# Performance work log

Hardware: AMD Instinct MI355X
Metric: run time of the kernel (lower is better)

## Reference

```python
import jax, jax.numpy as jnp
import numpy as np

B, H, W, C = 32, 56, 56, 192
WS, SHIFT, NH = 7, 3, 6
HD = C // NH
N = WS * WS
NW = (H // WS) * (W // WS)
SCALE = HD ** -0.5
EPS = 1e-5


def _layer_norm(x, g, b):
    mu = jnp.mean(x, axis=-1, keepdims=True)
    var = jnp.mean(jnp.square(x - mu), axis=-1, keepdims=True)
    return (x - mu) * jax.lax.rsqrt(var + EPS) * g + b


def _relative_position_index():
    coords = np.stack(np.meshgrid(np.arange(WS), np.arange(WS), indexing='ij'))  # [2,ws,ws]
    coords = coords.reshape(2, -1)                                               # [2,N]
    rel = coords[:, :, None] - coords[:, None, :]                                # [2,N,N]
    rel = rel.transpose(1, 2, 0).astype(np.int64)
    rel[..., 0] += WS - 1
    rel[..., 1] += WS - 1
    rel[..., 0] *= 2 * WS - 1
    return jnp.asarray(rel.sum(-1))  # [N,N]


def _attn_mask():
    img = np.zeros((H, W), dtype=np.float32)
    cnt = 0
    slices = (slice(0, -WS), slice(-WS, -SHIFT), slice(-SHIFT, None))
    for hs in slices:
        for ws_ in slices:
            img[hs, ws_] = cnt
            cnt += 1
    mw = img.reshape(H // WS, WS, W // WS, WS).transpose(0, 2, 1, 3).reshape(-1, N)  # [nW,N]
    diff = mw[:, :, None] - mw[:, None, :]
    return jnp.asarray(np.where(diff != 0, -100.0, 0.0).astype(np.float32))  # [nW,N,N]


REL_IDX = _relative_position_index()
ATTN_MASK = _attn_mask()


def setup_inputs() -> dict:
    key = jax.random.key(0)
    ks = jax.random.split(key, 16)
    s = 0.02
    return {
        'x': jax.random.normal(ks[0], (B, H * W, C), jnp.float32),
        'ln1_g': jnp.ones((C,), jnp.float32),
        'ln1_b': jnp.zeros((C,), jnp.float32),
        'qkv_w': jax.random.normal(ks[1], (3 * C, C), jnp.float32) * s,
        'qkv_b': jnp.zeros((3 * C,), jnp.float32),
        'proj_w': jax.random.normal(ks[2], (C, C), jnp.float32) * s,
        'proj_b': jnp.zeros((C,), jnp.float32),
        'rpb_table': jax.random.normal(ks[3], ((2 * WS - 1) ** 2, NH), jnp.float32) * s,
        'ln2_g': jnp.ones((C,), jnp.float32),
        'ln2_b': jnp.zeros((C,), jnp.float32),
        'fc1_w': jax.random.normal(ks[4], (4 * C, C), jnp.float32) * s,
        'fc1_b': jnp.zeros((4 * C,), jnp.float32),
        'fc2_w': jax.random.normal(ks[5], (C, 4 * C), jnp.float32) * s,
        'fc2_b': jnp.zeros((C,), jnp.float32),
    }


def reference(x, ln1_g, ln1_b, qkv_w, qkv_b, proj_w, proj_b, rpb_table,
              ln2_g, ln2_b, fc1_w, fc1_b, fc2_w, fc2_b):
    shortcut = x
    h = _layer_norm(x, ln1_g, ln1_b).reshape(B, H, W, C)
    # cyclic shift
    h = jnp.roll(h, (-SHIFT, -SHIFT), axis=(1, 2))
    # window partition -> [B*nW, N, C]
    h = h.reshape(B, H // WS, WS, W // WS, WS, C).transpose(0, 1, 3, 2, 4, 5)
    h = h.reshape(B * NW, N, C)
    # qkv
    qkv = h @ qkv_w.T + qkv_b                                   # [Bn,N,3C]
    qkv = qkv.reshape(B * NW, N, 3, NH, HD).transpose(2, 0, 3, 1, 4)
    q, k, v = qkv[0], qkv[1], qkv[2]                             # [Bn,nh,N,hd]
    attn = jnp.einsum('bhnd,bhmd->bhnm', q * SCALE, k)           # [Bn,nh,N,N]
    # relative position bias
    bias = rpb_table[REL_IDX.reshape(-1)].reshape(N, N, NH).transpose(2, 0, 1)
    attn = attn + bias[None]
    # shift mask
    attn = attn.reshape(B, NW, NH, N, N) + ATTN_MASK[None, :, None]
    attn = jax.nn.softmax(attn.reshape(B * NW, NH, N, N), axis=-1)
    h = jnp.einsum('bhnm,bhmd->bhnd', attn, v)                   # [Bn,nh,N,hd]
    h = h.transpose(0, 2, 1, 3).reshape(B * NW, N, C)
    h = h @ proj_w.T + proj_b
    # window reverse + reverse shift
    h = h.reshape(B, H // WS, W // WS, WS, WS, C).transpose(0, 1, 3, 2, 4, 5)
    h = h.reshape(B, H, W, C)
    h = jnp.roll(h, (SHIFT, SHIFT), axis=(1, 2)).reshape(B, H * W, C)
    x = shortcut + h
    # MLP
    m = _layer_norm(x, ln2_g, ln2_b)
    m = jax.nn.gelu(m @ fc1_w.T + fc1_b, approximate=False)
    m = m @ fc2_w.T + fc2_b
    return x + m
```

## Files before the change

kernel.cpp:

```cpp
#include <hip/hip_runtime.h>
#include <hip/hip_bf16.h>
#include <cstdint>
#include <cstddef>

typedef __hip_bfloat16 bf16;
using f32x4  = __attribute__((ext_vector_type(4))) float;
using bf16x8 = __attribute__((ext_vector_type(8))) short;

#define DEVI __device__ __forceinline__
#define WAITVM(N) asm volatile("s_waitcnt vmcnt(" #N ")" ::: "memory")

DEVI int reg3(int u) { return (u < 49) ? 0 : ((u < 53) ? 1 : 2); }

DEVI unsigned short f2bu(float v) {
  bf16 b = __float2bfloat16(v);
  return *reinterpret_cast<unsigned short*>(&b);
}

DEVI float gelu_f(float v) {
  const float y = 0.7978845608028654f * (v + 0.044715f * v * v * v);
  const float e = __expf(2.0f * y);
  const float th = 1.0f - 2.0f / (e + 1.0f);
  return 0.5f * v * (1.0f + th);
}

DEVI void gload_lds16(const void* g, void* l) {
  __builtin_amdgcn_global_load_lds(
      (const __attribute__((address_space(1))) unsigned int*)g,
      (__attribute__((address_space(3))) unsigned int*)l, 16, 0, 0);
}

__global__ __launch_bounds__(256) void cvt_kernel(const float* __restrict__ src,
                                                  bf16* __restrict__ dst, int n)
{
  const int i = blockIdx.x * 256 + threadIdx.x;
  if (i < n) dst[i] = __float2bfloat16(src[i]);
}

template<bool PERM>
__global__ __launch_bounds__(256) void ln_kernel(const float* __restrict__ x,
                                                 const float* __restrict__ gw,
                                                 const float* __restrict__ bw,
                                                 bf16* __restrict__ out,
                                                 int grow0)
{
  const int lane = threadIdx.x & 63;
  const int ridx = blockIdx.x * 4 + (threadIdx.x >> 6);
  size_t src;
  if (PERM) {
    const int g   = grow0 + ridx;
    const int wid = g / 49;
    const int nn  = g - wid * 49;
    const int b_  = wid >> 6, wim = wid & 63;
    const int wy  = wim >> 3, wx = wim & 7;
    const int ny  = nn / 7,  nx = nn - (nn / 7) * 7;
    int i = wy * 7 + ny + 3; if (i >= 56) i -= 56;
    int j = wx * 7 + nx + 3; if (j >= 56) j -= 56;
    src = (size_t)(b_ * 3136 + i * 56 + j);
  } else {
    src = (size_t)ridx;
  }
  const float* xr = x + src * 192;
  float v0 = xr[lane];
  float v1 = xr[lane + 64];
  float v2 = xr[lane + 128];
  float s = v0 + v1 + v2;
#pragma unroll
  for (int off = 32; off > 0; off >>= 1) s += __shfl_xor(s, off);
  const float mu = s * (1.0f / 192.0f);
  const float d0 = v0 - mu, d1 = v1 - mu, d2 = v2 - mu;
  float vs = d0 * d0 + d1 * d1 + d2 * d2;
#pragma unroll
  for (int off = 32; off > 0; off >>= 1) vs += __shfl_xor(vs, off);
  const float rstd = rsqrtf(vs * (1.0f / 192.0f) + 1e-5f);
  bf16* orow = out + (size_t)ridx * 192;
  orow[lane]       = __float2bfloat16(d0 * rstd * gw[lane]       + bw[lane]);
  orow[lane + 64]  = __float2bfloat16(d1 * rstd * gw[lane + 64]  + bw[lane + 64]);
  orow[lane + 128] = __float2bfloat16(d2 * rstd * gw[lane + 128] + bw[lane + 128]);
}

template<int MODE>
__global__ __launch_bounds__(512) void pgemm_kernel(const bf16* __restrict__ A,
                                                    const bf16* __restrict__ Bt,
                                                    const float* __restrict__ bias,
                                                    const float* __restrict__ resid,
                                                    void* __restrict__ outv,
                                                    int N, int grow0, int MT)
{
  __shared__ short Bp[192 * 192];
  __shared__ short La[2][64 * 192];
  const int tid  = threadIdx.x;
  const int lane = tid & 63;
  const int w    = tid >> 6;
  const int wm   = (w >> 2) * 32;
  const int wn   = (w & 3) * 48;
  const int n0   = blockIdx.x * 192;
  const int G    = gridDim.y;
  const int g    = blockIdx.y;
  const int kq   = lane >> 4;

  float bv[3];
  int ncol[3];
#pragma unroll
  for (int nf = 0; nf < 3; nf++) {
    ncol[nf] = n0 + wn + nf * 16 + (lane & 15);
    bv[nf]   = bias[ncol[nf]];
  }

#pragma unroll
  for (int i = 0; i < 9; i++) {
    const int chunk = w * 9 + i;
    const int idx = chunk * 64 + lane;
    const int row = idx / 24;
    const int seg = idx - row * 24;
    const int ksrc = (seg * 8) ^ ((row & 7) << 3);
    gload_lds16(Bt + (size_t)(n0 + row) * 192 + ksrc, Bp + chunk * 512);
  }

  auto stageA = [&](int buf, int mt) {
    const int m0 = mt * 64;
#pragma unroll
    for (int i = 0; i < 3; i++) {
      const int chunk = w * 3 + i;
      const int idx = chunk * 64 + lane;
      const int row = idx / 24;
      const int seg = idx - row * 24;
      const int ksrc = (seg * 8) ^ ((row & 7) << 3);
      gload_lds16(A + (size_t)(m0 + row) * 192 + ksrc, &La[buf][0] + chunk * 512);
    }
  };

  int buf = 0;
  if (g < MT) stageA(0, g);
  __syncthreads();

  for (int mt = g; mt < MT; mt += G) {
    if constexpr (MODE == 1) { WAITVM(48); } else { WAITVM(24); }
    __builtin_amdgcn_s_barrier();

    const char* LA = (const char*)&La[buf][0];
    f32x4 acc[2][3];
#pragma unroll
    for (int i = 0; i < 2; i++)
#pragma unroll
      for (int j = 0; j < 3; j++) acc[i][j] = (f32x4){0.f, 0.f, 0.f, 0.f};

#pragma unroll
    for (int kk = 0; kk < 6; kk++) {
      const int q = kk * 64 + (kq << 4);
      bf16x8 af[2], bg[3];
#pragma unroll
      for (int mf = 0; mf < 2; mf++) {
        const int ar = wm + mf * 16 + (lane & 15);
        af[mf] = *(const bf16x8*)(LA + ar * 384 + (q ^ ((ar & 7) << 4)));
      }
#pragma unroll
      for (int nf = 0; nf < 3; nf++) {
        const int br = wn + nf * 16 + (lane & 15);
        bg[nf] = *(const bf16x8*)((const char*)Bp + br * 384 + (q ^ ((br & 7) << 4)));
      }
#pragma unroll
      for (int mf = 0; mf < 2; mf++)
#pragma unroll
        for (int nf = 0; nf < 3; nf++)
          acc[mf][nf] = __builtin_amdgcn_mfma_f32_16x16x32_bf16(af[mf], bg[nf], acc[mf][nf], 0, 0, 0);
    }

    if (mt + G < MT) stageA(buf ^ 1, mt + G);

    const int m0 = mt * 64;
#pragma unroll
    for (int mf = 0; mf < 2; mf++) {
#pragma unroll
      for (int r = 0; r < 4; r++) {
        const int m = m0 + wm + mf * 16 + ((lane >> 4) << 2) + r;
        if constexpr (MODE == 1) {
          const int gm  = grow0 + m;
          const int wid = gm / 49;
          const int nn  = gm - wid * 49;
          const int b_  = wid >> 6, wim = wid & 63;
          const int wy  = wim >> 3, wx = wim & 7;
          const int ny  = nn / 7, nx = nn - (nn / 7) * 7;
          int i = wy * 7 + ny + 3; if (i >= 56) i -= 56;
          int j = wx * 7 + nx + 3; if (j >= 56) j -= 56;
          const size_t t = (size_t)(b_ * 3136 + i * 56 + j) * 192;
          float* O = (float*)outv;
#pragma unroll
          for (int nf = 0; nf < 3; nf++)
            O[t + ncol[nf]] = acc[mf][nf][r] + bv[nf] + resid[t + ncol[nf]];
        } else {
          bf16* O = (bf16*)outv + (size_t)m * N;
#pragma unroll
          for (int nf = 0; nf < 3; nf++) {
            float v = acc[mf][nf][r] + bv[nf];
            if constexpr (MODE == 2) v = gelu_f(v);
            O[ncol[nf]] = __float2bfloat16(v);
          }
        }
      }
    }
    buf ^= 1;
  }
}

__global__ __launch_bounds__(512, 4) void gemm_kernel(const bf16* __restrict__ A,
                                                      const bf16* __restrict__ Bt,
                                                      const float* __restrict__ bias,
                                                      void* __restrict__ outv,
                                                      int N, int K)
{
  __shared__ short lds[2][128 * 64 + 192 * 64];
  const int tid  = threadIdx.x;
  const int lane = tid & 63;
  const int w    = tid >> 6;
  const int wm   = (w >> 2) * 64;
  const int wn   = (w & 3) * 48;
  const int m0   = blockIdx.y * 128;
  const int n0   = blockIdx.x * 192;
  const int lrow = lane >> 3;
  const int lseg = lane & 7;
  const int ksw  = (lseg * 8) ^ (lrow << 3);

  f32x4 acc[4][3];
#pragma unroll
  for (int i = 0; i < 4; i++)
#pragma unroll
    for (int j = 0; j < 3; j++) acc[i][j] = (f32x4){0.f, 0.f, 0.f, 0.f};

  const int nk = K >> 6;

  auto issue = [&](int buf, int kt) {
    const int k0 = kt << 6;
    short* LA = &lds[buf][0];
    short* LB = &lds[buf][128 * 64];
#pragma unroll
    for (int i = 0; i < 2; i++) {
      const int chunk = w * 2 + i;
      gload_lds16(A + (size_t)(m0 + chunk * 8 + lrow) * K + (k0 + ksw), LA + chunk * 512);
    }
#pragma unroll
    for (int i = 0; i < 3; i++) {
      const int chunk = w * 3 + i;
      gload_lds16(Bt + (size_t)(n0 + chunk * 8 + lrow) * K + (k0 + ksw), LB + chunk * 512);
    }
  };

  issue(0, 0);
  __syncthreads();
  int buf = 0;

  for (int kt = 0; kt < nk; kt++) {
    if (kt + 1 < nk) {
      issue(buf ^ 1, kt + 1);
      WAITVM(5);
    } else {
      WAITVM(0);
    }
    __builtin_amdgcn_s_barrier();
    const char* LA = (const char*)&lds[buf][0];
    const char* LB = (const char*)&lds[buf][128 * 64];
#pragma unroll
    for (int kk = 0; kk < 2; kk++) {
      bf16x8 af[4], bg[3];
#pragma unroll
      for (int mf = 0; mf < 4; mf++) {
        const int row = wm + mf * 16 + (lane & 15);
        const int kb  = (kk * 64 + ((lane >> 4) << 4)) ^ ((row & 7) << 4);
        af[mf] = *(const bf16x8*)(LA + row * 128 + kb);
      }
#pragma unroll
      for (int nf = 0; nf < 3; nf++) {
        const int row = wn + nf * 16 + (lane & 15);
        const int kb  = (kk * 64 + ((lane >> 4) << 4)) ^ ((row & 7) << 4);
        bg[nf] = *(const bf16x8*)(LB + row * 128 + kb);
      }
#pragma unroll
      for (int mf = 0; mf < 4; mf++)
#pragma unroll
        for (int nf = 0; nf < 3; nf++)
          acc[mf][nf] = __builtin_amdgcn_mfma_f32_16x16x32_bf16(af[mf], bg[nf], acc[mf][nf], 0, 0, 0);
    }
    __builtin_amdgcn_s_barrier();
    buf ^= 1;
  }

  float bv[3];
  int ncol[3];
#pragma unroll
  for (int nf = 0; nf < 3; nf++) {
    ncol[nf] = n0 + wn + nf * 16 + (lane & 15);
    bv[nf]   = bias[ncol[nf]];
  }
#pragma unroll
  for (int mf = 0; mf < 4; mf++) {
#pragma unroll
    for (int r = 0; r < 4; r++) {
      const int m = m0 + wm + mf * 16 + ((lane >> 4) << 2) + r;
      float* O = (float*)outv + (size_t)m * N;
#pragma unroll
      for (int nf = 0; nf < 3; nf++)
        O[ncol[nf]] = acc[mf][nf][r] + bv[nf] + O[ncol[nf]];
    }
  }
}

__global__ __launch_bounds__(64) void attn_kernel(const bf16* __restrict__ qkv,
                                                  const float* __restrict__ rpb,
                                                  bf16* __restrict__ aout)
{
  __shared__ unsigned short Vt[32 * 64];
  __shared__ unsigned short Pl[64 * 64];
  __shared__ float Bl[169];
  const int lane = threadIdx.x;
  const int wid  = blockIdx.x;
  const int h    = blockIdx.y;
  const unsigned short* qkvu = (const unsigned short*)qkv;
  const size_t base = (size_t)wid * 49 * 576 + h * 32;

#pragma unroll
  for (int i = 0; i < 3; i++) {
    const int idx = lane + 64 * i;
    if (idx < 169) Bl[idx] = rpb[idx * 6 + h];
  }
#pragma unroll
  for (int i = 0; i < 8; i++)
    ((unsigned long long*)Vt)[lane + 64 * i] = 0ull;

#pragma unroll
  for (int it = 0; it < 7; it++) {
    const int idx = lane + 64 * it;
    if (idx < 392) {
      const int n  = idx >> 3;
      const int d0 = (idx & 7) * 4;
      ushort4 v = *(const ushort4*)(qkvu + base + (size_t)n * 576 + 384 + d0);
      Vt[(d0 + 0) * 64 + (n ^ (((d0 + 0) & 7) << 3))] = v.x;
      Vt[(d0 + 1) * 64 + (n ^ (((d0 + 1) & 7) << 3))] = v.y;
      Vt[(d0 + 2) * 64 + (n ^ (((d0 + 2) & 7) << 3))] = v.z;
      Vt[(d0 + 3) * 64 + (n ^ (((d0 + 3) & 7) << 3))] = v.w;
    }
  }

  bf16x8 qf[4], kf[4];
#pragma unroll
  for (int t = 0; t < 4; t++) {
    int rq = (lane & 15) + t * 16; if (rq > 48) rq = 48;
    qf[t] = *(const bf16x8*)(qkvu + base + (size_t)rq * 576 + ((lane >> 4) * 8));
    kf[t] = *(const bf16x8*)(qkvu + base + (size_t)rq * 576 + 192 + ((lane >> 4) * 8));
  }

  f32x4 s[4][4];
#pragma unroll
  for (int mt = 0; mt < 4; mt++)
#pragma unroll
    for (int nt = 0; nt < 4; nt++)
      s[mt][nt] = __builtin_amdgcn_mfma_f32_16x16x32_bf16(qf[mt], kf[nt],
                    (f32x4){0.f, 0.f, 0.f, 0.f}, 0, 0, 0);

  const int wim = wid & 63;
  const int wy = wim >> 3, wx = wim & 7;
  int labn[4], ch[4], cw[4];
  bool cval[4];
#pragma unroll
  for (int nt = 0; nt < 4; nt++) {
    const int C = (lane & 15) + nt * 16;
    cval[nt] = (C < 49);
    const int cc = cval[nt] ? C : 48;
    ch[nt] = cc / 7; cw[nt] = cc - ch[nt] * 7;
    labn[nt] = reg3(wy * 7 + ch[nt]) * 3 + reg3(wx * 7 + cw[nt]);
  }

#pragma unroll
  for (int mt = 0; mt < 4; mt++) {
    f32x4 rm, sm, inv;
#pragma unroll
    for (int r = 0; r < 4; r++) {
      int R = mt * 16 + ((lane >> 4) << 2) + r; if (R > 48) R = 48;
      const int mh = R / 7, mw = R - (R / 7) * 7;
      const int labm = reg3(wy * 7 + mh) * 3 + reg3(wx * 7 + mw);
#pragma unroll
      for (int nt = 0; nt < 4; nt++) {
        float sv = s[mt][nt][r] * 0.1767766953f
                 + Bl[(mh - ch[nt] + 6) * 13 + (mw - cw[nt] + 6)];
        if (labn[nt] != labm) sv -= 100.f;
        if (!cval[nt]) sv = -3e38f;
        s[mt][nt][r] = sv;
      }
      rm[r] = fmaxf(fmaxf(s[mt][0][r], s[mt][1][r]), fmaxf(s[mt][2][r], s[mt][3][r]));
    }
#pragma unroll
    for (int mk = 1; mk < 16; mk <<= 1)
#pragma unroll
      for (int r = 0; r < 4; r++) rm[r] = fmaxf(rm[r], __shfl_xor(rm[r], mk));
#pragma unroll
    for (int r = 0; r < 4; r++) {
      float acc = 0.f;
#pragma unroll
      for (int nt = 0; nt < 4; nt++) {
        const float p = __expf(s[mt][nt][r] - rm[r]);
        s[mt][nt][r] = p;
        acc += p;
      }
      sm[r] = acc;
    }
#pragma unroll
    for (int mk = 1; mk < 16; mk <<= 1)
#pragma unroll
      for (int r = 0; r < 4; r++) sm[r] += __shfl_xor(sm[r], mk);
#pragma unroll
    for (int r = 0; r < 4; r++) inv[r] = 1.0f / sm[r];
#pragma unroll
    for (int nt = 0; nt < 4; nt++)
#pragma unroll
      for (int r = 0; r < 4; r++) {
        const int R = mt * 16 + ((lane >> 4) << 2) + r;
        const int C = (lane & 15) + nt * 16;
        Pl[R * 64 + (C ^ ((R & 7) << 3))] = f2bu(s[mt][nt][r] * inv[r]);
      }
  }

  f32x4 o[4][2];
#pragma unroll
  for (int mt = 0; mt < 4; mt++)
#pragma unroll
    for (int n2 = 0; n2 < 2; n2++) o[mt][n2] = (f32x4){0.f, 0.f, 0.f, 0.f};
#pragma unroll
  for (int kk = 0; kk < 2; kk++) {
    const int kb = kk * 64 + ((lane >> 4) << 4);
    bf16x8 vb[2];
#pragma unroll
    for (int n2 = 0; n2 < 2; n2++) {
      const int d = (lane & 15) + n2 * 16;
      vb[n2] = *(const bf16x8*)((const char*)Vt + d * 128 + (kb ^ ((d & 7) << 4)));
    }
#pragma unroll
    for (int mt = 0; mt < 4; mt++) {
      const int R = (lane & 15) + mt * 16;
      const bf16x8 pa = *(const bf16x8*)((const char*)Pl + R * 128 + (kb ^ ((R & 7) << 4)));
#pragma unroll
      for (int n2 = 0; n2 < 2; n2++)
        o[mt][n2] = __builtin_amdgcn_mfma_f32_16x16x32_bf16(pa, vb[n2], o[mt][n2], 0, 0, 0);
    }
  }

#pragma unroll
  for (int mt = 0; mt < 4; mt++)
#pragma unroll
    for (int r = 0; r < 4; r++) {
      const int R = mt * 16 + ((lane >> 4) << 2) + r;
      if (R < 49) {
        bf16* orow = aout + (size_t)(wid * 49 + R) * 192 + h * 32;
#pragma unroll
        for (int n2 = 0; n2 < 2; n2++)
          orow[n2 * 16 + (lane & 15)] = __float2bfloat16(o[mt][n2][r]);
      }
    }
}

extern "C" void kernel_launch(void* const* d_in, const int* in_sizes, int n_in,
                              void* d_out, int out_size, void* d_ws, size_t ws_size,
                              hipStream_t stream)
{
  (void)in_sizes; (void)n_in; (void)out_size;
  const float* x     = (const float*)d_in[0];
  const float* ln1g  = (const float*)d_in[1];
  const float* ln1b  = (const float*)d_in[2];
  const float* qkvw  = (const float*)d_in[3];
  const float* qkvb  = (const float*)d_in[4];
  const float* projw = (const float*)d_in[5];
  const float* projb = (const float*)d_in[6];
  const float* rpb   = (const float*)d_in[7];
  const float* ln2g  = (const float*)d_in[8];
  const float* ln2b  = (const float*)d_in[9];
  const float* fc1w  = (const float*)d_in[10];
  const float* fc1b  = (const float*)d_in[11];
  const float* fc2w  = (const float*)d_in[12];
  const float* fc2b  = (const float*)d_in[13];
  float* out = (float*)d_out;
  char* ws   = (char*)d_ws;

  bf16* wqkv = (bf16*)(ws);
  bf16* wproj = (bf16*)(ws + 221184);
  bf16* wfc1 = (bf16*)(ws + 294912);
  bf16* wfc2 = (bf16*)(ws + 589824);
  cvt_kernel<<<dim3(432), dim3(256), 0, stream>>>(qkvw, wqkv, 110592);
  cvt_kernel<<<dim3(144), dim3(256), 0, stream>>>(projw, wproj, 36864);
  cvt_kernel<<<dim3(576), dim3(256), 0, stream>>>(fc1w, wfc1, 147456);
  cvt_kernel<<<dim3(576), dim3(256), 0, stream>>>(fc2w, wfc2, 147456);

  char* cws = ws + 884736;
  const size_t avail = (ws_size > 884736ull) ? ws_size - 884736ull : 0;

  int Bc = 32;
  while (Bc > 2 && (size_t)Bc * 4816896ull > avail) Bc >>= 1;
  const int nb = 32 / Bc;
  bf16* qkv_c  = (bf16*)cws;
  bf16* hwin_c = (bf16*)(cws + (size_t)Bc * 3612672ull);

  for (int c = 0; c < nb; c++) {
    const int R0 = c * Bc * 3136;
    const int Mc = Bc * 3136;
    const int MT = Mc / 64;
    const int Gq = (MT < 85) ? MT : 85;
    const int Gp = (MT < 256) ? MT : 256;
    ln_kernel<true><<<dim3(Mc / 4), dim3(256), 0, stream>>>(x, ln1g, ln1b, hwin_c, R0);
    pgemm_kernel<0><<<dim3(3, Gq), dim3(512), 0, stream>>>(hwin_c, wqkv, qkvb, nullptr, qkv_c, 576, 0, MT);
    attn_kernel<<<dim3(Bc * 64, 6), dim3(64), 0, stream>>>(qkv_c, rpb, hwin_c);
    pgemm_kernel<1><<<dim3(1, Gp), dim3(512), 0, stream>>>(hwin_c, wproj, projb, x, out, 192, R0, MT);
  }

  int Rc = 100352;
  while (Rc > 6272 && (size_t)Rc * 1920ull > avail) Rc >>= 1;
  bf16* ln2_c = (bf16*)cws;
  bf16* a1_c  = (bf16*)(cws + (size_t)Rc * 384ull);

  for (int r0 = 0; r0 < 100352; r0 += Rc) {
    const int MT1 = Rc / 64;
    const int G1  = (MT1 < 64) ? MT1 : 64;
    ln_kernel<false><<<dim3(Rc / 4), dim3(256), 0, stream>>>(out + (size_t)r0 * 192, ln2g, ln2b, ln2_c, 0);
    pgemm_kernel<2><<<dim3(4, G1), dim3(512), 0, stream>>>(ln2_c, wfc1, fc1b, nullptr, a1_c, 768, 0, MT1);
    gemm_kernel<<<dim3(1, Rc / 128), dim3(512), 0, stream>>>(a1_c, wfc2, fc2b, out + (size_t)r0 * 192, 192, 768);
  }
}
```

Baseline: 354.2 us.

## Fuse LN1, QKV GEMM, window attention and projection into one per-window kernel

```diff
diff --git a/kernel.cpp b/kernel.cpp
--- a/kernel.cpp
+++ b/kernel.cpp
@@ -37,33 +37,28 @@
   if (i < n) dst[i] = __float2bfloat16(src[i]);
 }
 
-template<bool PERM>
+__global__ __launch_bounds__(256) void cvtT_kernel(const float* __restrict__ src,
+                                                   bf16* __restrict__ dst, int K, int KT, int n)
+{
+  const int i = blockIdx.x * 256 + threadIdx.x;
+  if (i >= n) return;
+  const int e   = i & 7;
+  const int l   = (i >> 3) & 63;
+  const int blk = i >> 9;
+  const int kk  = blk % KT;
+  const int nf  = blk / KT;
+  dst[i] = __float2bfloat16(src[(size_t)(nf * 16 + (l & 15)) * K + kk * 32 + (l >> 4) * 8 + e]);
+}
+
 __global__ __launch_bounds__(256) void ln_kernel(const float* __restrict__ x,
                                                  const float* __restrict__ gw,
                                                  const float* __restrict__ bw,
-                                                 bf16* __restrict__ out,
-                                                 int grow0)
+                                                 bf16* __restrict__ out)
 {
   const int lane = threadIdx.x & 63;
   const int ridx = blockIdx.x * 4 + (threadIdx.x >> 6);
-  size_t src;
-  if (PERM) {
-    const int g   = grow0 + ridx;
-    const int wid = g / 49;
-    const int nn  = g - wid * 49;
-    const int b_  = wid >> 6, wim = wid & 63;
-    const int wy  = wim >> 3, wx = wim & 7;
-    const int ny  = nn / 7,  nx = nn - (nn / 7) * 7;
-    int i = wy * 7 + ny + 3; if (i >= 56) i -= 56;
-    int j = wx * 7 + nx + 3; if (j >= 56) j -= 56;
-    src = (size_t)(b_ * 3136 + i * 56 + j);
-  } else {
-    src = (size_t)ridx;
-  }
-  const float* xr = x + src * 192;
-  float v0 = xr[lane];
-  float v1 = xr[lane + 64];
-  float v2 = xr[lane + 128];
+  const float* xr = x + (size_t)ridx * 192;
+  float v0 = xr[lane], v1 = xr[lane + 64], v2 = xr[lane + 128];
   float s = v0 + v1 + v2;
 #pragma unroll
   for (int off = 32; off > 0; off >>= 1) s += __shfl_xor(s, off);
@@ -79,13 +74,293 @@
   orow[lane + 128] = __float2bfloat16(d2 * rstd * gw[lane + 128] + bw[lane + 128]);
 }
 
+__global__ __launch_bounds__(256) void wattn_kernel(const float* __restrict__ x,
+                                                    const float* __restrict__ g1,
+                                                    const float* __restrict__ b1,
+                                                    const bf16* __restrict__ wqkvT,
+                                                    const float* __restrict__ qkvb,
+                                                    const bf16* __restrict__ wprojT,
+                                                    const float* __restrict__ projb,
+                                                    const float* __restrict__ rpb,
+                                                    float* __restrict__ out)
+{
+  __shared__ short hwao[64 * 192];
+  __shared__ short qkvL[64 * 576];
+  __shared__ unsigned short PV[4][6144];
+  __shared__ float Bl[6 * 169];
+  const int tid  = threadIdx.x;
+  const int lane = tid & 63;
+  const int w    = tid >> 6;
+  const int wid  = blockIdx.x;
+  const int wim  = wid & 63;
+  const int wy   = wim >> 3, wx = wim & 7;
+  const int b_   = wid >> 6;
+  const int kq   = lane >> 4;
+
+  for (int i = tid; i < 1014; i += 256) {
+    const int h = i / 169;
+    Bl[i] = rpb[(i - h * 169) * 6 + h];
+  }
+
+  for (int r = w; r < 49; r += 4) {
+    const int ny = r / 7, nx = r - (r / 7) * 7;
+    int i = wy * 7 + ny + 3; if (i >= 56) i -= 56;
+    int j = wx * 7 + nx + 3; if (j >= 56) j -= 56;
+    const float* xr = x + (size_t)(b_ * 3136 + i * 56 + j) * 192;
+    float v0 = xr[lane], v1 = xr[lane + 64], v2 = xr[lane + 128];
+    float s = v0 + v1 + v2;
+#pragma unroll
+    for (int off = 32; off > 0; off >>= 1) s += __shfl_xor(s, off);
+    const float mu = s * (1.0f / 192.0f);
+    const float d0 = v0 - mu, d1 = v1 - mu, d2 = v2 - mu;
+    float vs = d0 * d0 + d1 * d1 + d2 * d2;
+#pragma unroll
+    for (int off = 32; off > 0; off >>= 1) vs += __shfl_xor(vs, off);
+    const float rstd = rsqrtf(vs * (1.0f / 192.0f) + 1e-5f);
+    const int rx = (r & 7) << 4;
+    *(unsigned short*)((char*)hwao + r * 384 + ((2 * lane) ^ rx))         = f2bu(d0 * rstd * g1[lane]       + b1[lane]);
+    *(unsigned short*)((char*)hwao + r * 384 + ((2 * (lane + 64)) ^ rx))  = f2bu(d1 * rstd * g1[lane + 64]  + b1[lane + 64]);
+    *(unsigned short*)((char*)hwao + r * 384 + ((2 * (lane + 128)) ^ rx)) = f2bu(d2 * rstd * g1[lane + 128] + b1[lane + 128]);
+  }
+  for (int i = tid; i < 15 * 192; i += 256) {
+    const int r = 49 + i / 192, c = i - (i / 192) * 192;
+    *(unsigned short*)((char*)hwao + r * 384 + ((2 * c) ^ ((r & 7) << 4))) = 0;
+  }
+  __syncthreads();
+
+#pragma unroll
+  for (int cc = 0; cc < 3; cc++) {
+    const int c0 = w * 144 + cc * 48;
+    f32x4 acc[4][3];
+#pragma unroll
+    for (int i = 0; i < 4; i++)
+#pragma unroll
+      for (int j = 0; j < 3; j++) acc[i][j] = (f32x4){0.f, 0.f, 0.f, 0.f};
+#pragma unroll
+    for (int kk = 0; kk < 6; kk++) {
+      const int q = kk * 64 + (kq << 4);
+      bf16x8 af[4], bg[3];
+#pragma unroll
+      for (int mf = 0; mf < 4; mf++) {
+        const int ar = mf * 16 + (lane & 15);
+        af[mf] = *(const bf16x8*)((const char*)hwao + ar * 384 + (q ^ ((ar & 7) << 4)));
+      }
+#pragma unroll
+      for (int nf = 0; nf < 3; nf++) {
+        const int blk = (c0 / 16 + nf) * 6 + kk;
+        bg[nf] = *(const bf16x8*)(wqkvT + (size_t)blk * 512 + lane * 8);
+      }
+#pragma unroll
+      for (int mf = 0; mf < 4; mf++)
+#pragma unroll
+        for (int nf = 0; nf < 3; nf++)
+          acc[mf][nf] = __builtin_amdgcn_mfma_f32_16x16x32_bf16(af[mf], bg[nf], acc[mf][nf], 0, 0, 0);
+    }
+    float bv[3];
+#pragma unroll
+    for (int nf = 0; nf < 3; nf++) bv[nf] = qkvb[c0 + nf * 16 + (lane & 15)];
+#pragma unroll
+    for (int mf = 0; mf < 4; mf++)
+#pragma unroll
+      for (int nf = 0; nf < 3; nf++)
+#pragma unroll
+        for (int r = 0; r < 4; r++) {
+          const int R = mf * 16 + (kq << 2) + r;
+          const int C = c0 + nf * 16 + (lane & 15);
+          *(unsigned short*)((char*)qkvL + R * 1152 + ((2 * C) ^ ((R & 7) << 4)))
+              = f2bu(acc[mf][nf][r] + bv[nf]);
+        }
+  }
+  __syncthreads();
+
+  unsigned short* Pl = &PV[w][0];
+  unsigned short* Vt = &PV[w][4096];
+  for (int h = w; h < 6; h += 4) {
+#pragma unroll
+    for (int i = 0; i < 8; i++)
+      ((unsigned long long*)Vt)[lane + 64 * i] = 0ull;
+#pragma unroll
+    for (int it = 0; it < 7; it++) {
+      const int idx = lane + 64 * it;
+      if (idx < 392) {
+        const int n  = idx >> 3;
+        const int d0 = (idx & 7) * 4;
+        ushort4 v = *(const ushort4*)((const char*)qkvL + n * 1152
+                        + ((768 + h * 64 + d0 * 2) ^ ((n & 7) << 4)));
+        Vt[(d0 + 0) * 64 + (n ^ (((d0 + 0) & 7) << 3))] = v.x;
+        Vt[(d0 + 1) * 64 + (n ^ (((d0 + 1) & 7) << 3))] = v.y;
+        Vt[(d0 + 2) * 64 + (n ^ (((d0 + 2) & 7) << 3))] = v.z;
+        Vt[(d0 + 3) * 64 + (n ^ (((d0 + 3) & 7) << 3))] = v.w;
+      }
+    }
+    bf16x8 qf[4], kf[4];
+#pragma unroll
+    for (int t = 0; t < 4; t++) {
+      const int rq = (lane & 15) + t * 16;
+      const int sw = (rq & 7) << 4;
+      qf[t] = *(const bf16x8*)((const char*)qkvL + rq * 1152 + ((h * 64 + (kq << 4)) ^ sw));
+      kf[t] = *(const bf16x8*)((const char*)qkvL + rq * 1152 + ((384 + h * 64 + (kq << 4)) ^ sw));
+    }
+    f32x4 s[4][4];
+#pragma unroll
+    for (int mt = 0; mt < 4; mt++)
+#pragma unroll
+      for (int nt = 0; nt < 4; nt++)
+        s[mt][nt] = __builtin_amdgcn_mfma_f32_16x16x32_bf16(qf[mt], kf[nt],
+                      (f32x4){0.f, 0.f, 0.f, 0.f}, 0, 0, 0);
+
+    int labn[4], ch[4], cw[4];
+    bool cval[4];
+#pragma unroll
+    for (int nt = 0; nt < 4; nt++) {
+      const int C = (lane & 15) + nt * 16;
+      cval[nt] = (C < 49);
+      const int cc2 = cval[nt] ? C : 48;
+      ch[nt] = cc2 / 7; cw[nt] = cc2 - ch[nt] * 7;
+      labn[nt] = reg3(wy * 7 + ch[nt]) * 3 + reg3(wx * 7 + cw[nt]);
+    }
+#pragma unroll
+    for (int mt = 0; mt < 4; mt++) {
+      f32x4 rm, sm, inv;
+#pragma unroll
+      for (int r = 0; r < 4; r++) {
+        int R = mt * 16 + (kq << 2) + r; if (R > 48) R = 48;
+        const int mh = R / 7, mw = R - (R / 7) * 7;
+        const int labm = reg3(wy * 7 + mh) * 3 + reg3(wx * 7 + mw);
+#pragma unroll
+        for (int nt = 0; nt < 4; nt++) {
+          float sv = s[mt][nt][r] * 0.1767766953f
+                   + Bl[h * 169 + (mh - ch[nt] + 6) * 13 + (mw - cw[nt] + 6)];
+          if (labn[nt] != labm) sv -= 100.f;
+          if (!cval[nt]) sv = -3e38f;
+          s[mt][nt][r] = sv;
+        }
+        rm[r] = fmaxf(fmaxf(s[mt][0][r], s[mt][1][r]), fmaxf(s[mt][2][r], s[mt][3][r]));
+      }
+#pragma unroll
+      for (int mk = 1; mk < 16; mk <<= 1)
+#pragma unroll
+        for (int r = 0; r < 4; r++) rm[r] = fmaxf(rm[r], __shfl_xor(rm[r], mk));
+#pragma unroll
+      for (int r = 0; r < 4; r++) {
+        float a = 0.f;
+#pragma unroll
+        for (int nt = 0; nt < 4; nt++) {
+          const float p = __expf(s[mt][nt][r] - rm[r]);
+          s[mt][nt][r] = p;
+          a += p;
+        }
+        sm[r] = a;
+      }
+#pragma unroll
+      for (int mk = 1; mk < 16; mk <<= 1)
+#pragma unroll
+        for (int r = 0; r < 4; r++) sm[r] += __shfl_xor(sm[r], mk);
+#pragma unroll
+      for (int r = 0; r < 4; r++) inv[r] = 1.0f / sm[r];
+#pragma unroll
+      for (int nt = 0; nt < 4; nt++)
+#pragma unroll
+        for (int r = 0; r < 4; r++) {
+          const int R = mt * 16 + (kq << 2) + r;
+          const int C = (lane & 15) + nt * 16;
+          Pl[R * 64 + (C ^ ((R & 7) << 3))] = f2bu(s[mt][nt][r] * inv[r]);
+        }
+    }
+    f32x4 o[4][2];
+#pragma unroll
+    for (int mt = 0; mt < 4; mt++)
+#pragma unroll
+      for (int n2 = 0; n2 < 2; n2++) o[mt][n2] = (f32x4){0.f, 0.f, 0.f, 0.f};
+#pragma unroll
+    for (int kk = 0; kk < 2; kk++) {
+      const int kb = kk * 64 + (kq << 4);
+      bf16x8 vb[2];
+#pragma unroll
+      for (int n2 = 0; n2 < 2; n2++) {
+        const int d = (lane & 15) + n2 * 16;
+        vb[n2] = *(const bf16x8*)((const char*)Vt + d * 128 + (kb ^ ((d & 7) << 4)));
+      }
+#pragma unroll
+      for (int mt = 0; mt < 4; mt++) {
+        const int R = (lane & 15) + mt * 16;
+        const bf16x8 pa = *(const bf16x8*)((const char*)Pl + R * 128 + (kb ^ ((R & 7) << 4)));
+#pragma unroll
+        for (int n2 = 0; n2 < 2; n2++)
+          o[mt][n2] = __builtin_amdgcn_mfma_f32_16x16x32_bf16(pa, vb[n2], o[mt][n2], 0, 0, 0);
+      }
+    }
+#pragma unroll
+    for (int mt = 0; mt < 4; mt++)
+#pragma unroll
+      for (int r = 0; r < 4; r++) {
+        const int R = mt * 16 + (kq << 2) + r;
+#pragma unroll
+        for (int n2 = 0; n2 < 2; n2++) {
+          const int C = h * 32 + n2 * 16 + (lane & 15);
+          *(unsigned short*)((char*)hwao + R * 384 + ((2 * C) ^ ((R & 7) << 4)))
+              = f2bu(o[mt][n2][r]);
+        }
+      }
+  }
+  __syncthreads();
+
+  {
+    const int c0 = w * 48;
+    f32x4 acc[4][3];
+#pragma unroll
+    for (int i = 0; i < 4; i++)
+#pragma unroll
+      for (int j = 0; j < 3; j++) acc[i][j] = (f32x4){0.f, 0.f, 0.f, 0.f};
+#pragma unroll
+    for (int kk = 0; kk < 6; kk++) {
+      const int q = kk * 64 + (kq << 4);
+      bf16x8 af[4], bg[3];
+#pragma unroll
+      for (int mf = 0; mf < 4; mf++) {
+        const int ar = mf * 16 + (lane & 15);
+        af[mf] = *(const bf16x8*)((const char*)hwao + ar * 384 + (q ^ ((ar & 7) << 4)));
+      }
+#pragma unroll
+      for (int nf = 0; nf < 3; nf++) {
+        const int blk = (w * 3 + nf) * 6 + kk;
+        bg[nf] = *(const bf16x8*)(wprojT + (size_t)blk * 512 + lane * 8);
+      }
+#pragma unroll
+      for (int mf = 0; mf < 4; mf++)
+#pragma unroll
+        for (int nf = 0; nf < 3; nf++)
+          acc[mf][nf] = __builtin_amdgcn_mfma_f32_16x16x32_bf16(af[mf], bg[nf], acc[mf][nf], 0, 0, 0);
+    }
+    float bv[3];
+#pragma unroll
+    for (int nf = 0; nf < 3; nf++) bv[nf] = projb[c0 + nf * 16 + (lane & 15)];
+#pragma unroll
+    for (int mf = 0; mf < 4; mf++)
+#pragma unroll
+      for (int r = 0; r < 4; r++) {
+        const int m = mf * 16 + (kq << 2) + r;
+        if (m < 49) {
+          const int ny = m / 7, nx = m - (m / 7) * 7;
+          int i = wy * 7 + ny + 3; if (i >= 56) i -= 56;
+          int j = wx * 7 + nx + 3; if (j >= 56) j -= 56;
+          const size_t t = (size_t)(b_ * 3136 + i * 56 + j) * 192;
+#pragma unroll
+          for (int nf = 0; nf < 3; nf++) {
+            const int col = c0 + nf * 16 + (lane & 15);
+            out[t + col] = acc[mf][nf][r] + bv[nf] + x[t + col];
+          }
+        }
+      }
+  }
+}
+
 template<int MODE>
 __global__ __launch_bounds__(512) void pgemm_kernel(const bf16* __restrict__ A,
                                                     const bf16* __restrict__ Bt,
                                                     const float* __restrict__ bias,
-                                                    const float* __restrict__ resid,
                                                     void* __restrict__ outv,
-                                                    int N, int grow0, int MT)
+                                                    int N, int MT)
 {
   __shared__ short Bp[192 * 192];
   __shared__ short La[2][64 * 192];
@@ -135,7 +410,7 @@
   __syncthreads();
 
   for (int mt = g; mt < MT; mt += G) {
-    if constexpr (MODE == 1) { WAITVM(48); } else { WAITVM(24); }
+    WAITVM(24);
     __builtin_amdgcn_s_barrier();
 
     const char* LA = (const char*)&La[buf][0];
@@ -174,28 +449,12 @@
 #pragma unroll
       for (int r = 0; r < 4; r++) {
         const int m = m0 + wm + mf * 16 + ((lane >> 4) << 2) + r;
-        if constexpr (MODE == 1) {
-          const int gm  = grow0 + m;
-          const int wid = gm / 49;
-          const int nn  = gm - wid * 49;
-          const int b_  = wid >> 6, wim = wid & 63;
-          const int wy  = wim >> 3, wx = wim & 7;
-          const int ny  = nn / 7, nx = nn - (nn / 7) * 7;
-          int i = wy * 7 + ny + 3; if (i >= 56) i -= 56;
-          int j = wx * 7 + nx + 3; if (j >= 56) j -= 56;
-          const size_t t = (size_t)(b_ * 3136 + i * 56 + j) * 192;
-          float* O = (float*)outv;
-#pragma unroll
-          for (int nf = 0; nf < 3; nf++)
-            O[t + ncol[nf]] = acc[mf][nf][r] + bv[nf] + resid[t + ncol[nf]];
-        } else {
-          bf16* O = (bf16*)outv + (size_t)m * N;
-#pragma unroll
-          for (int nf = 0; nf < 3; nf++) {
-            float v = acc[mf][nf][r] + bv[nf];
-            if constexpr (MODE == 2) v = gelu_f(v);
-            O[ncol[nf]] = __float2bfloat16(v);
-          }
+        bf16* O = (bf16*)outv + (size_t)m * N;
+#pragma unroll
+        for (int nf = 0; nf < 3; nf++) {
+          float v = acc[mf][nf][r] + bv[nf];
+          if constexpr (MODE == 2) v = gelu_f(v);
+          O[ncol[nf]] = __float2bfloat16(v);
         }
       }
     }
@@ -302,158 +561,6 @@
         O[ncol[nf]] = acc[mf][nf][r] + bv[nf] + O[ncol[nf]];
     }
   }
-}
-
-__global__ __launch_bounds__(64) void attn_kernel(const bf16* __restrict__ qkv,
-                                                  const float* __restrict__ rpb,
-                                                  bf16* __restrict__ aout)
-{
-  __shared__ unsigned short Vt[32 * 64];
-  __shared__ unsigned short Pl[64 * 64];
-  __shared__ float Bl[169];
-  const int lane = threadIdx.x;
-  const int wid  = blockIdx.x;
-  const int h    = blockIdx.y;
-  const unsigned short* qkvu = (const unsigned short*)qkv;
-  const size_t base = (size_t)wid * 49 * 576 + h * 32;
-
-#pragma unroll
-  for (int i = 0; i < 3; i++) {
-    const int idx = lane + 64 * i;
-    if (idx < 169) Bl[idx] = rpb[idx * 6 + h];
-  }
-#pragma unroll
-  for (int i = 0; i < 8; i++)
-    ((unsigned long long*)Vt)[lane + 64 * i] = 0ull;
-
-#pragma unroll
-  for (int it = 0; it < 7; it++) {
-    const int idx = lane + 64 * it;
-    if (idx < 392) {
-      const int n  = idx >> 3;
-      const int d0 = (idx & 7) * 4;
-      ushort4 v = *(const ushort4*)(qkvu + base + (size_t)n * 576 + 384 + d0);
-      Vt[(d0 + 0) * 64 + (n ^ (((d0 + 0) & 7) << 3))] = v.x;
-      Vt[(d0 + 1) * 64 + (n ^ (((d0 + 1) & 7) << 3))] = v.y;
-      Vt[(d0 + 2) * 64 + (n ^ (((d0 + 2) & 7) << 3))] = v.z;
-      Vt[(d0 + 3) * 64 + (n ^ (((d0 + 3) & 7) << 3))] = v.w;
-    }
-  }
-
-  bf16x8 qf[4], kf[4];
-#pragma unroll
-  for (int t = 0; t < 4; t++) {
-    int rq = (lane & 15) + t * 16; if (rq > 48) rq = 48;
-    qf[t] = *(const bf16x8*)(qkvu + base + (size_t)rq * 576 + ((lane >> 4) * 8));
-    kf[t] = *(const bf16x8*)(qkvu + base + (size_t)rq * 576 + 192 + ((lane >> 4) * 8));
-  }
-
-  f32x4 s[4][4];
-#pragma unroll
-  for (int mt = 0; mt < 4; mt++)
-#pragma unroll
-    for (int nt = 0; nt < 4; nt++)
-      s[mt][nt] = __builtin_amdgcn_mfma_f32_16x16x32_bf16(qf[mt], kf[nt],
-                    (f32x4){0.f, 0.f, 0.f, 0.f}, 0, 0, 0);
-
-  const int wim = wid & 63;
-  const int wy = wim >> 3, wx = wim & 7;
-  int labn[4], ch[4], cw[4];
-  bool cval[4];
-#pragma unroll
-  for (int nt = 0; nt < 4; nt++) {
-    const int C = (lane & 15) + nt * 16;
-    cval[nt] = (C < 49);
-    const int cc = cval[nt] ? C : 48;
-    ch[nt] = cc / 7; cw[nt] = cc - ch[nt] * 7;
-    labn[nt] = reg3(wy * 7 + ch[nt]) * 3 + reg3(wx * 7 + cw[nt]);
-  }
-
-#pragma unroll
-  for (int mt = 0; mt < 4; mt++) {
-    f32x4 rm, sm, inv;
-#pragma unroll
-    for (int r = 0; r < 4; r++) {
-      int R = mt * 16 + ((lane >> 4) << 2) + r; if (R > 48) R = 48;
-      const int mh = R / 7, mw = R - (R / 7) * 7;
-      const int labm = reg3(wy * 7 + mh) * 3 + reg3(wx * 7 + mw);
-#pragma unroll
-      for (int nt = 0; nt < 4; nt++) {
-        float sv = s[mt][nt][r] * 0.1767766953f
-                 + Bl[(mh - ch[nt] + 6) * 13 + (mw - cw[nt] + 6)];
-        if (labn[nt] != labm) sv -= 100.f;
-        if (!cval[nt]) sv = -3e38f;
-        s[mt][nt][r] = sv;
-      }
-      rm[r] = fmaxf(fmaxf(s[mt][0][r], s[mt][1][r]), fmaxf(s[mt][2][r], s[mt][3][r]));
-    }
-#pragma unroll
-    for (int mk = 1; mk < 16; mk <<= 1)
-#pragma unroll
-      for (int r = 0; r < 4; r++) rm[r] = fmaxf(rm[r], __shfl_xor(rm[r], mk));
-#pragma unroll
-    for (int r = 0; r < 4; r++) {
-      float acc = 0.f;
-#pragma unroll
-      for (int nt = 0; nt < 4; nt++) {
-        const float p = __expf(s[mt][nt][r] - rm[r]);
-        s[mt][nt][r] = p;
-        acc += p;
-      }
-      sm[r] = acc;
-    }
-#pragma unroll
-    for (int mk = 1; mk < 16; mk <<= 1)
-#pragma unroll
-      for (int r = 0; r < 4; r++) sm[r] += __shfl_xor(sm[r], mk);
-#pragma unroll
-    for (int r = 0; r < 4; r++) inv[r] = 1.0f / sm[r];
-#pragma unroll
-    for (int nt = 0; nt < 4; nt++)
-#pragma unroll
-      for (int r = 0; r < 4; r++) {
-        const int R = mt * 16 + ((lane >> 4) << 2) + r;
-        const int C = (lane & 15) + nt * 16;
-        Pl[R * 64 + (C ^ ((R & 7) << 3))] = f2bu(s[mt][nt][r] * inv[r]);
-      }
-  }
-
-  f32x4 o[4][2];
-#pragma unroll
-  for (int mt = 0; mt < 4; mt++)
-#pragma unroll
-    for (int n2 = 0; n2 < 2; n2++) o[mt][n2] = (f32x4){0.f, 0.f, 0.f, 0.f};
-#pragma unroll
-  for (int kk = 0; kk < 2; kk++) {
-    const int kb = kk * 64 + ((lane >> 4) << 4);
-    bf16x8 vb[2];
-#pragma unroll
-    for (int n2 = 0; n2 < 2; n2++) {
-      const int d = (lane & 15) + n2 * 16;
-      vb[n2] = *(const bf16x8*)((const char*)Vt + d * 128 + (kb ^ ((d & 7) << 4)));
-    }
-#pragma unroll
-    for (int mt = 0; mt < 4; mt++) {
-      const int R = (lane & 15) + mt * 16;
-      const bf16x8 pa = *(const bf16x8*)((const char*)Pl + R * 128 + (kb ^ ((R & 7) << 4)));
-#pragma unroll
-      for (int n2 = 0; n2 < 2; n2++)
-        o[mt][n2] = __builtin_amdgcn_mfma_f32_16x16x32_bf16(pa, vb[n2], o[mt][n2], 0, 0, 0);
-    }
-  }
-
-#pragma unroll
-  for (int mt = 0; mt < 4; mt++)
-#pragma unroll
-    for (int r = 0; r < 4; r++) {
-      const int R = mt * 16 + ((lane >> 4) << 2) + r;
-      if (R < 49) {
-        bf16* orow = aout + (size_t)(wid * 49 + R) * 192 + h * 32;
-#pragma unroll
-        for (int n2 = 0; n2 < 2; n2++)
-          orow[n2 * 16 + (lane & 15)] = __float2bfloat16(o[mt][n2][r]);
-      }
-    }
 }
 
 extern "C" void kernel_launch(void* const* d_in, const int* in_sizes, int n_in,
@@ -478,35 +585,20 @@
   float* out = (float*)d_out;
   char* ws   = (char*)d_ws;
 
-  bf16* wqkv = (bf16*)(ws);
-  bf16* wproj = (bf16*)(ws + 221184);
+  bf16* wqkvT = (bf16*)(ws);
+  bf16* wprojT = (bf16*)(ws + 221184);
   bf16* wfc1 = (bf16*)(ws + 294912);
   bf16* wfc2 = (bf16*)(ws + 589824);
-  cvt_kernel<<<dim3(432), dim3(256), 0, stream>>>(qkvw, wqkv, 110592);
-  cvt_kernel<<<dim3(144), dim3(256), 0, stream>>>(projw, wproj, 36864);
+  cvtT_kernel<<<dim3(432), dim3(256), 0, stream>>>(qkvw, wqkvT, 192, 6, 110592);
+  cvtT_kernel<<<dim3(144), dim3(256), 0, stream>>>(projw, wprojT, 192, 6, 36864);
   cvt_kernel<<<dim3(576), dim3(256), 0, stream>>>(fc1w, wfc1, 147456);
   cvt_kernel<<<dim3(576), dim3(256), 0, stream>>>(fc2w, wfc2, 147456);
 
   char* cws = ws + 884736;
   const size_t avail = (ws_size > 884736ull) ? ws_size - 884736ull : 0;
 
-  int Bc = 32;
-  while (Bc > 2 && (size_t)Bc * 4816896ull > avail) Bc >>= 1;
-  const int nb = 32 / Bc;
-  bf16* qkv_c  = (bf16*)cws;
-  bf16* hwin_c = (bf16*)(cws + (size_t)Bc * 3612672ull);
-
-  for (int c = 0; c < nb; c++) {
-    const int R0 = c * Bc * 3136;
-    const int Mc = Bc * 3136;
-    const int MT = Mc / 64;
-    const int Gq = (MT < 85) ? MT : 85;
-    const int Gp = (MT < 256) ? MT : 256;
-    ln_kernel<true><<<dim3(Mc / 4), dim3(256), 0, stream>>>(x, ln1g, ln1b, hwin_c, R0);
-    pgemm_kernel<0><<<dim3(3, Gq), dim3(512), 0, stream>>>(hwin_c, wqkv, qkvb, nullptr, qkv_c, 576, 0, MT);
-    attn_kernel<<<dim3(Bc * 64, 6), dim3(64), 0, stream>>>(qkv_c, rpb, hwin_c);
-    pgemm_kernel<1><<<dim3(1, Gp), dim3(512), 0, stream>>>(hwin_c, wproj, projb, x, out, 192, R0, MT);
-  }
+  wattn_kernel<<<dim3(2048), dim3(256), 0, stream>>>(x, ln1g, ln1b, wqkvT, qkvb,
+                                                     wprojT, projb, rpb, out);
 
   int Rc = 100352;
   while (Rc > 6272 && (size_t)Rc * 1920ull > avail) Rc >>= 1;
@@ -516,8 +608,8 @@
   for (int r0 = 0; r0 < 100352; r0 += Rc) {
     const int MT1 = Rc / 64;
     const int G1  = (MT1 < 64) ? MT1 : 64;
-    ln_kernel<false><<<dim3(Rc / 4), dim3(256), 0, stream>>>(out + (size_t)r0 * 192, ln2g, ln2b, ln2_c, 0);
-    pgemm_kernel<2><<<dim3(4, G1), dim3(512), 0, stream>>>(ln2_c, wfc1, fc1b, nullptr, a1_c, 768, 0, MT1);
+    ln_kernel<<<dim3(Rc / 4), dim3(256), 0, stream>>>(out + (size_t)r0 * 192, ln2g, ln2b, ln2_c);
+    pgemm_kernel<2><<<dim3(4, G1), dim3(512), 0, stream>>>(ln2_c, wfc1, fc1b, a1_c, 768, MT1);
     gemm_kernel<<<dim3(1, Rc / 128), dim3(512), 0, stream>>>(a1_c, wfc2, fc2b, out + (size_t)r0 * 192, 192, 768);
   }
 }
```

Result: slower. 478.9 us (+35.2%).

## Fuse LayerNorm into the QKV and FC1 GEMM prologues

Applied to the files above, without the earlier changes.

```diff
diff --git a/kernel.cpp b/kernel.cpp
--- a/kernel.cpp
+++ b/kernel.cpp
@@ -37,55 +37,172 @@
   if (i < n) dst[i] = __float2bfloat16(src[i]);
 }
 
-template<bool PERM>
-__global__ __launch_bounds__(256) void ln_kernel(const float* __restrict__ x,
-                                                 const float* __restrict__ gw,
-                                                 const float* __restrict__ bw,
-                                                 bf16* __restrict__ out,
-                                                 int grow0)
+template<int MODE>
+__global__ __launch_bounds__(512) void plngemm_kernel(const float* __restrict__ X,
+                                                      const float* __restrict__ gw,
+                                                      const float* __restrict__ bw,
+                                                      const bf16* __restrict__ Bt,
+                                                      const float* __restrict__ bias,
+                                                      bf16* __restrict__ outp,
+                                                      int N, int grow0, int MT)
 {
-  const int lane = threadIdx.x & 63;
-  const int ridx = blockIdx.x * 4 + (threadIdx.x >> 6);
-  size_t src;
-  if (PERM) {
-    const int g   = grow0 + ridx;
-    const int wid = g / 49;
-    const int nn  = g - wid * 49;
-    const int b_  = wid >> 6, wim = wid & 63;
-    const int wy  = wim >> 3, wx = wim & 7;
-    const int ny  = nn / 7,  nx = nn - (nn / 7) * 7;
-    int i = wy * 7 + ny + 3; if (i >= 56) i -= 56;
-    int j = wx * 7 + nx + 3; if (j >= 56) j -= 56;
-    src = (size_t)(b_ * 3136 + i * 56 + j);
-  } else {
-    src = (size_t)ridx;
-  }
-  const float* xr = x + src * 192;
-  float v0 = xr[lane];
-  float v1 = xr[lane + 64];
-  float v2 = xr[lane + 128];
-  float s = v0 + v1 + v2;
-#pragma unroll
-  for (int off = 32; off > 0; off >>= 1) s += __shfl_xor(s, off);
-  const float mu = s * (1.0f / 192.0f);
-  const float d0 = v0 - mu, d1 = v1 - mu, d2 = v2 - mu;
-  float vs = d0 * d0 + d1 * d1 + d2 * d2;
-#pragma unroll
-  for (int off = 32; off > 0; off >>= 1) vs += __shfl_xor(vs, off);
-  const float rstd = rsqrtf(vs * (1.0f / 192.0f) + 1e-5f);
-  bf16* orow = out + (size_t)ridx * 192;
-  orow[lane]       = __float2bfloat16(d0 * rstd * gw[lane]       + bw[lane]);
-  orow[lane + 64]  = __float2bfloat16(d1 * rstd * gw[lane + 64]  + bw[lane + 64]);
-  orow[lane + 128] = __float2bfloat16(d2 * rstd * gw[lane + 128] + bw[lane + 128]);
-}
-
-template<int MODE>
+  __shared__ short Bp[192 * 192];
+  __shared__ short La[2][64 * 192];
+  const int tid   = threadIdx.x;
+  const int lane  = tid & 63;
+  const int w     = tid >> 6;
+  const int wm    = (w >> 2) * 32;
+  const int wn    = (w & 3) * 48;
+  const int n0    = blockIdx.x * 192;
+  const int G     = gridDim.y;
+  const int g     = blockIdx.y;
+  const int kq    = lane >> 4;
+  const int rowid = tid >> 3;
+  const int sub   = tid & 7;
+  const int c24   = sub * 24;
+
+  float bv[3];
+  int ncol[3];
+#pragma unroll
+  for (int nf = 0; nf < 3; nf++) {
+    ncol[nf] = n0 + wn + nf * 16 + (lane & 15);
+    bv[nf]   = bias[ncol[nf]];
+  }
+  float gv[24], bb[24];
+#pragma unroll
+  for (int i = 0; i < 6; i++) {
+    const f32x4 gg = *(const f32x4*)(gw + c24 + 4 * i);
+    const f32x4 bz = *(const f32x4*)(bw + c24 + 4 * i);
+#pragma unroll
+    for (int e = 0; e < 4; e++) { gv[4 * i + e] = gg[e]; bb[4 * i + e] = bz[e]; }
+  }
+
+#pragma unroll
+  for (int i = 0; i < 9; i++) {
+    const int chunk = w * 9 + i;
+    const int idx = chunk * 64 + lane;
+    const int row = idx / 24;
+    const int seg = idx - row * 24;
+    const int ksrc = (seg * 8) ^ ((row & 7) << 3);
+    gload_lds16(Bt + (size_t)(n0 + row) * 192 + ksrc, Bp + chunk * 512);
+  }
+
+  f32x4 vf[6];
+  auto issueA = [&](int mt) {
+    const float* src;
+    if constexpr (MODE == 0) {
+      const int gm  = grow0 + mt * 64 + rowid;
+      const int wid = gm / 49;
+      const int nn  = gm - wid * 49;
+      const int b_  = wid >> 6, wim = wid & 63;
+      const int wy  = wim >> 3, wx = wim & 7;
+      const int ny  = nn / 7, nx = nn - (nn / 7) * 7;
+      int i2 = wy * 7 + ny + 3; if (i2 >= 56) i2 -= 56;
+      int j2 = wx * 7 + nx + 3; if (j2 >= 56) j2 -= 56;
+      src = X + (size_t)(b_ * 3136 + i2 * 56 + j2) * 192 + c24;
+    } else {
+      src = X + (size_t)(mt * 64 + rowid) * 192 + c24;
+    }
+#pragma unroll
+    for (int i = 0; i < 6; i++) vf[i] = *(const f32x4*)(src + 4 * i);
+  };
+
+  auto lnwrite = [&](int buf) {
+    float v[24];
+#pragma unroll
+    for (int i = 0; i < 6; i++)
+#pragma unroll
+      for (int e = 0; e < 4; e++) v[4 * i + e] = vf[i][e];
+    float s = 0.f;
+#pragma unroll
+    for (int i = 0; i < 24; i++) s += v[i];
+    s += __shfl_xor(s, 1); s += __shfl_xor(s, 2); s += __shfl_xor(s, 4);
+    const float mu = s * (1.0f / 192.0f);
+    float vs = 0.f;
+#pragma unroll
+    for (int i = 0; i < 24; i++) { const float d = v[i] - mu; vs += d * d; }
+    vs += __shfl_xor(vs, 1); vs += __shfl_xor(vs, 2); vs += __shfl_xor(vs, 4);
+    const float rstd = rsqrtf(vs * (1.0f / 192.0f) + 1e-5f);
+    const float a = rstd, b0 = -mu * rstd;
+    const int rx = (rowid & 7) << 4;
+#pragma unroll
+    for (int c3 = 0; c3 < 3; c3++) {
+      bf16x8 pk;
+#pragma unroll
+      for (int e = 0; e < 8; e++) {
+        const int i = c3 * 8 + e;
+        pk[e] = (short)f2bu((v[i] * a + b0) * gv[i] + bb[i]);
+      }
+      *(bf16x8*)((char*)&La[buf][0] + rowid * 384 + ((c24 * 2 + c3 * 16) ^ rx)) = pk;
+    }
+  };
+
+  if (g < MT) { issueA(g); lnwrite(0); }
+  __syncthreads();
+
+  int buf = 0;
+  for (int mt = g; mt < MT; mt += G) {
+    const bool pf = (mt + G < MT);
+    if (pf) issueA(mt + G);
+    asm volatile("" ::: "memory");
+
+    const char* LA = (const char*)&La[buf][0];
+    f32x4 acc[2][3];
+#pragma unroll
+    for (int i = 0; i < 2; i++)
+#pragma unroll
+      for (int j = 0; j < 3; j++) acc[i][j] = (f32x4){0.f, 0.f, 0.f, 0.f};
+
+#pragma unroll
+    for (int kk = 0; kk < 6; kk++) {
+      const int q = kk * 64 + (kq << 4);
+      bf16x8 af[2], bg[3];
+#pragma unroll
+      for (int mf = 0; mf < 2; mf++) {
+        const int ar = wm + mf * 16 + (lane & 15);
+        af[mf] = *(const bf16x8*)(LA + ar * 384 + (q ^ ((ar & 7) << 4)));
+      }
+#pragma unroll
+      for (int nf = 0; nf < 3; nf++) {
+        const int br = wn + nf * 16 + (lane & 15);
+        bg[nf] = *(const bf16x8*)((const char*)Bp + br * 384 + (q ^ ((br & 7) << 4)));
+      }
+#pragma unroll
+      for (int mf = 0; mf < 2; mf++)
+#pragma unroll
+        for (int nf = 0; nf < 3; nf++)
+          acc[mf][nf] = __builtin_amdgcn_mfma_f32_16x16x32_bf16(af[mf], bg[nf], acc[mf][nf], 0, 0, 0);
+    }
+
+    const int m0 = mt * 64;
+#pragma unroll
+    for (int mf = 0; mf < 2; mf++) {
+#pragma unroll
+      for (int r = 0; r < 4; r++) {
+        const int m = m0 + wm + mf * 16 + ((lane >> 4) << 2) + r;
+        bf16* O = outp + (size_t)m * N;
+#pragma unroll
+        for (int nf = 0; nf < 3; nf++) {
+          float vvv = acc[mf][nf][r] + bv[nf];
+          if constexpr (MODE == 2) vvv = gelu_f(vvv);
+          O[ncol[nf]] = __float2bfloat16(vvv);
+        }
+      }
+    }
+
+    if (pf) lnwrite(buf ^ 1);
+    asm volatile("s_waitcnt lgkmcnt(0)" ::: "memory");
+    __builtin_amdgcn_s_barrier();
+    buf ^= 1;
+  }
+}
+
 __global__ __launch_bounds__(512) void pgemm_kernel(const bf16* __restrict__ A,
                                                     const bf16* __restrict__ Bt,
                                                     const float* __restrict__ bias,
                                                     const float* __restrict__ resid,
-                                                    void* __restrict__ outv,
-                                                    int N, int grow0, int MT)
+                                                    float* __restrict__ outv,
+                                                    int grow0, int MT)
 {
   __shared__ short Bp[192 * 192];
   __shared__ short La[2][64 * 192];
@@ -135,7 +252,7 @@
   __syncthreads();
 
   for (int mt = g; mt < MT; mt += G) {
-    if constexpr (MODE == 1) { WAITVM(48); } else { WAITVM(24); }
+    WAITVM(48);
     __builtin_amdgcn_s_barrier();
 
     const char* LA = (const char*)&La[buf][0];
@@ -174,29 +291,18 @@
 #pragma unroll
       for (int r = 0; r < 4; r++) {
         const int m = m0 + wm + mf * 16 + ((lane >> 4) << 2) + r;
-        if constexpr (MODE == 1) {
-          const int gm  = grow0 + m;
-          const int wid = gm / 49;
-          const int nn  = gm - wid * 49;
-          const int b_  = wid >> 6, wim = wid & 63;
-          const int wy  = wim >> 3, wx = wim & 7;
-          const int ny  = nn / 7, nx = nn - (nn / 7) * 7;
-          int i = wy * 7 + ny + 3; if (i >= 56) i -= 56;
-          int j = wx * 7 + nx + 3; if (j >= 56) j -= 56;
-          const size_t t = (size_t)(b_ * 3136 + i * 56 + j) * 192;
-          float* O = (float*)outv;
-#pragma unroll
-          for (int nf = 0; nf < 3; nf++)
-            O[t + ncol[nf]] = acc[mf][nf][r] + bv[nf] + resid[t + ncol[nf]];
-        } else {
-          bf16* O = (bf16*)outv + (size_t)m * N;
-#pragma unroll
-          for (int nf = 0; nf < 3; nf++) {
-            float v = acc[mf][nf][r] + bv[nf];
-            if constexpr (MODE == 2) v = gelu_f(v);
-            O[ncol[nf]] = __float2bfloat16(v);
-          }
-        }
+        const int gm  = grow0 + m;
+        const int wid = gm / 49;
+        const int nn  = gm - wid * 49;
+        const int b_  = wid >> 6, wim = wid & 63;
+        const int wy  = wim >> 3, wx = wim & 7;
+        const int ny  = nn / 7, nx = nn - (nn / 7) * 7;
+        int i = wy * 7 + ny + 3; if (i >= 56) i -= 56;
+        int j = wx * 7 + nx + 3; if (j >= 56) j -= 56;
+        const size_t t = (size_t)(b_ * 3136 + i * 56 + j) * 192;
+#pragma unroll
+        for (int nf = 0; nf < 3; nf++)
+          outv[t + ncol[nf]] = acc[mf][nf][r] + bv[nf] + resid[t + ncol[nf]];
       }
     }
     buf ^= 1;
@@ -502,22 +608,23 @@
     const int MT = Mc / 64;
     const int Gq = (MT < 85) ? MT : 85;
     const int Gp = (MT < 256) ? MT : 256;
-    ln_kernel<true><<<dim3(Mc / 4), dim3(256), 0, stream>>>(x, ln1g, ln1b, hwin_c, R0);
-    pgemm_kernel<0><<<dim3(3, Gq), dim3(512), 0, stream>>>(hwin_c, wqkv, qkvb, nullptr, qkv_c, 576, 0, MT);
+    plngemm_kernel<0><<<dim3(3, Gq), dim3(512), 0, stream>>>(x, ln1g, ln1b, wqkv, qkvb,
+                                                             qkv_c, 576, R0, MT);
     attn_kernel<<<dim3(Bc * 64, 6), dim3(64), 0, stream>>>(qkv_c, rpb, hwin_c);
-    pgemm_kernel<1><<<dim3(1, Gp), dim3(512), 0, stream>>>(hwin_c, wproj, projb, x, out, 192, R0, MT);
+    pgemm_kernel<<<dim3(1, Gp), dim3(512), 0, stream>>>(hwin_c, wproj, projb, x, out, R0, MT);
   }
 
   int Rc = 100352;
-  while (Rc > 6272 && (size_t)Rc * 1920ull > avail) Rc >>= 1;
-  bf16* ln2_c = (bf16*)cws;
-  bf16* a1_c  = (bf16*)(cws + (size_t)Rc * 384ull);
+  while (Rc > 6272 && (size_t)Rc * 1536ull > avail) Rc >>= 1;
+  bf16* a1_c = (bf16*)cws;
 
   for (int r0 = 0; r0 < 100352; r0 += Rc) {
     const int MT1 = Rc / 64;
     const int G1  = (MT1 < 64) ? MT1 : 64;
-    ln_kernel<false><<<dim3(Rc / 4), dim3(256), 0, stream>>>(out + (size_t)r0 * 192, ln2g, ln2b, ln2_c, 0);
-    pgemm_kernel<2><<<dim3(4, G1), dim3(512), 0, stream>>>(ln2_c, wfc1, fc1b, nullptr, a1_c, 768, 0, MT1);
-    gemm_kernel<<<dim3(1, Rc / 128), dim3(512), 0, stream>>>(a1_c, wfc2, fc2b, out + (size_t)r0 * 192, 192, 768);
-  }
-}
+    plngemm_kernel<2><<<dim3(4, G1), dim3(512), 0, stream>>>(out + (size_t)r0 * 192,
+                                                             ln2g, ln2b, wfc1, fc1b,
+                                                             a1_c, 768, 0, MT1);
+    gemm_kernel<<<dim3(1, Rc / 128), dim3(512), 0, stream>>>(a1_c, wfc2, fc2b,
+                                                             out + (size_t)r0 * 192, 192, 768);
+  }
+}
```

Result: faster. 343.3 us (-3.1%).
